# Kernel optimization log

Measured on AMD Instinct MI355X. Metric: run time of the kernel, lower is better.

## Reference

```python
import jax, jax.numpy as jnp
import numpy as np

H = 1024        # hidden_size == voc.num_words (required by module math)
V_OUT = 32000   # output_size / embedding vocab
B = 128
S = 512
MOG = 5


def _p(key, shape, scale=0.02):
    return scale * jax.random.normal(key, shape, dtype=jnp.float32)


def setup_inputs() -> dict:
    key = jax.random.key(0)
    ks = jax.random.split(key, 24)
    inp = {
        "input_step": jax.random.randint(ks[0], (1, B), 0, V_OUT),
        "encoder_outputs": jax.random.normal(ks[1], (S, B, H), dtype=jnp.float32),
        "h1": jax.random.normal(ks[2], (B, H), dtype=jnp.float32),
        "c1": jax.random.normal(ks[3], (B, H), dtype=jnp.float32),
        "emb": _p(ks[4], (V_OUT, H), 1.0),
        # mogrifier + LSTMCell params, layer 1 (input_size == hidden_size == H)
        "mog1_W": _p(ks[5], (MOG, H, H)),
        "mog1_b": _p(ks[6], (MOG, H)),
        "lstm1_Wih": _p(ks[7], (4 * H, H)),
        "lstm1_Whh": _p(ks[8], (4 * H, H)),
        "lstm1_bih": _p(ks[9], (4 * H,)),
        "lstm1_bhh": _p(ks[10], (4 * H,)),
        # layer 2
        "mog2_W": _p(ks[11], (MOG, H, H)),
        "mog2_b": _p(ks[12], (MOG, H)),
        "lstm2_Wih": _p(ks[13], (4 * H, H)),
        "lstm2_Whh": _p(ks[14], (4 * H, H)),
        "lstm2_bih": _p(ks[15], (4 * H,)),
        "lstm2_bhh": _p(ks[16], (4 * H,)),
        # MogLSTM.fc: hidden -> voc.num_words (== H)
        "fc_W": _p(ks[17], (H, H)),
        "fc_b": _p(ks[18], (H,)),
        # decoder concat / out
        "concat_W": _p(ks[19], (H, 2 * H)),
        "concat_b": _p(ks[20], (H,)),
        "out_W": _p(ks[21], (V_OUT, H)),
        "out_b": _p(ks[22], (V_OUT,)),
    }
    return inp


def _mog_lstm_cell(x, h, c, mog_W, mog_b, Wih, Whh, bih, bhh):
    # mogrify: 5 alternating tiny gated updates (x first, then h, ...)
    for i in range(MOG):
        g = 2.0 * jax.nn.sigmoid((h if (i + 1) % 2 != 0 else x) @ mog_W[i].T + mog_b[i])
        if (i + 1) % 2 == 0:
            h = g * h
        else:
            x = g * x
    gates = x @ Wih.T + bih + h @ Whh.T + bhh          # [B, 4H]
    i_, f_, g_, o_ = jnp.split(gates, 4, axis=1)        # torch order: i,f,g,o
    c = jax.nn.sigmoid(f_) * c + jax.nn.sigmoid(i_) * jnp.tanh(g_)
    h = jax.nn.sigmoid(o_) * jnp.tanh(c)
    return h, c


def reference(input_step, encoder_outputs, h1, c1, emb,
              mog1_W, mog1_b, lstm1_Wih, lstm1_Whh, lstm1_bih, lstm1_bhh,
              mog2_W, mog2_b, lstm2_Wih, lstm2_Whh, lstm2_bih, lstm2_bhh,
              fc_W, fc_b, concat_W, concat_b, out_W, out_b):
    x = emb[input_step[0]]                               # [B, H] (seq_len = 1)
    # MogLSTM: layer-1 uses provided (h1, c1); layer-2 state is zero-init
    h1n, _ = _mog_lstm_cell(x, h1, c1, mog1_W, mog1_b,
                            lstm1_Wih, lstm1_Whh, lstm1_bih, lstm1_bhh)
    z = jnp.zeros_like(h1n)
    h2n, _ = _mog_lstm_cell(h1n, z, z, mog2_W, mog2_b,
                            lstm2_Wih, lstm2_Whh, lstm2_bih, lstm2_bhh)
    rnn_out = h2n @ fc_W.T + fc_b                        # [B, H] (fc -> voc.num_words == H)
    hidden = h2n[None]                                   # [1, B, H]
    # Luong dot attention over encoder memory [S, B, H]
    scores = jnp.einsum('bh,sbh->bs', rnn_out, encoder_outputs)
    attn = jax.nn.softmax(scores, axis=1)                # [B, S]
    context = jnp.einsum('bs,sbh->bh', attn, encoder_outputs)
    concat_out = jnp.tanh(jnp.concatenate([rnn_out, context], axis=1) @ concat_W.T + concat_b)
    output = jax.nn.softmax(concat_out @ out_W.T + out_b, axis=1)  # [B, V_OUT]
    return output, hidden
```

## Files before the change

### kernel.cpp

```cpp
#include <hip/hip_runtime.h>
#include <math.h>

typedef unsigned short u16;
typedef unsigned int   u32;

#define B    128
#define H    1024
#define SEQ  512
#define VOUT 32000

#define NQ   4
#define SQB  (SEQ / NQ)
#define TS   8
#define NT   (SQB / TS)

using bf16x8 = __attribute__((ext_vector_type(8))) short;
using f32x4  = __attribute__((ext_vector_type(4))) float;

__device__ __forceinline__ float b2f(u32 u){ return __uint_as_float((u & 0xffffu) << 16); }
__device__ __forceinline__ float sigm(float x){ return 1.0f / (1.0f + expf(-x)); }
__device__ __forceinline__ u32 cvt2(float a, float b){
  u32 ua = __float_as_uint(a); ua += 0x7fffu + ((ua >> 16) & 1u);
  u32 ub = __float_as_uint(b); ub += 0x7fffu + ((ub >> 16) & 1u);
  return (ua >> 16) | (ub & 0xffff0000u);
}

__device__ __forceinline__ float ldf(const void* p, size_t i, int bf){
  return bf ? b2f(((const u16*)p)[i]) : ((const float*)p)[i];
}

__global__ void k_detect(const u16* __restrict__ enc, int* __restrict__ flag){
  __shared__ int cnt;
  if (threadIdx.x == 0) cnt = 0;
  __syncthreads();
  int c = 0;
  for (int j = threadIdx.x; j < 512; j += 256){
    u32 u = enc[j];
    u32 e = (u >> 7) & 0xFFu;
    c += (u == 0u || (e >= 100u && e <= 130u)) ? 1 : 0;
  }
  atomicAdd(&cnt, c);
  __syncthreads();
  if (threadIdx.x == 0) *flag = (cnt > 410) ? 1 : 0;
}

__global__ void k_init(const int* __restrict__ idx, const void* __restrict__ emb,
                       const void* __restrict__ h1, float* __restrict__ X, float* __restrict__ Hb,
                       const int* __restrict__ flagp){
  int bf = *flagp;
  int t = blockIdx.x * 256 + threadIdx.x;
  int b = t >> 10, h = t & (H - 1);
  X[t]  = ldf(emb, (size_t)idx[b] * H + h, bf);
  Hb[t] = ldf(h1, t, bf);
}

template<int OUT>
__global__ __launch_bounds__(256)
void gemm_s(const float* __restrict__ A, const void* __restrict__ W, size_t wOff,
            float* __restrict__ P, int K, int Kc, int N, const int* __restrict__ flagp)
{
  const int bf = *flagp;
  __shared__ float As[32][132];
  __shared__ float Wt[32][68];
  const int t  = threadIdx.x;
  const int n0 = blockIdx.x * 64;
  const int kbase = blockIdx.y * Kc;
  const int sb = t >> 1,  sk = (t & 1) << 4;
  const int wn = t >> 2,  wk = (t & 3) << 3;
  const int bx = (t & 15) << 3;
  const int ny = (t >> 4) << 2;

  float acc[8][4];
  #pragma unroll
  for (int i = 0; i < 8; ++i)
    #pragma unroll
    for (int j = 0; j < 4; ++j) acc[i][j] = 0.f;

  for (int k0 = 0; k0 < Kc; k0 += 32){
    const int kb = kbase + k0;
    const float4* Ap = (const float4*)(A + (size_t)sb * K + kb + sk);
    float4 a0 = Ap[0], a1 = Ap[1], a2 = Ap[2], a3 = Ap[3];
    size_t we = wOff + (size_t)(n0 + wn) * K + kb + wk;
    float w0,w1,w2,w3,w4,w5,w6,w7;
    if (bf){
      uint4 wv = *(const uint4*)((const u16*)W + we);
      w0=b2f(wv.x); w1=b2f(wv.x>>16); w2=b2f(wv.y); w3=b2f(wv.y>>16);
      w4=b2f(wv.z); w5=b2f(wv.z>>16); w6=b2f(wv.w); w7=b2f(wv.w>>16);
    } else {
      const float* Wf = (const float*)W + we;
      float4 p = *(const float4*)Wf, q = *(const float4*)(Wf + 4);
      w0=p.x; w1=p.y; w2=p.z; w3=p.w; w4=q.x; w5=q.y; w6=q.z; w7=q.w;
    }

    As[sk+ 0][sb]=a0.x; As[sk+ 1][sb]=a0.y; As[sk+ 2][sb]=a0.z; As[sk+ 3][sb]=a0.w;
    As[sk+ 4][sb]=a1.x; As[sk+ 5][sb]=a1.y; As[sk+ 6][sb]=a1.z; As[sk+ 7][sb]=a1.w;
    As[sk+ 8][sb]=a2.x; As[sk+ 9][sb]=a2.y; As[sk+10][sb]=a2.z; As[sk+11][sb]=a2.w;
    As[sk+12][sb]=a3.x; As[sk+13][sb]=a3.y; As[sk+14][sb]=a3.z; As[sk+15][sb]=a3.w;
    Wt[wk+0][wn]=w0; Wt[wk+1][wn]=w1; Wt[wk+2][wn]=w2; Wt[wk+3][wn]=w3;
    Wt[wk+4][wn]=w4; Wt[wk+5][wn]=w5; Wt[wk+6][wn]=w6; Wt[wk+7][wn]=w7;
    __syncthreads();

    #pragma unroll
    for (int kk = 0; kk < 32; ++kk){
      float4 wv = *(const float4*)(&Wt[kk][ny]);
      float a[8];
      #pragma unroll
      for (int i = 0; i < 8; ++i) a[i] = As[kk][bx+i];
      #pragma unroll
      for (int i = 0; i < 8; ++i){
        acc[i][0] = fmaf(a[i], wv.x, acc[i][0]);
        acc[i][1] = fmaf(a[i], wv.y, acc[i][1]);
        acc[i][2] = fmaf(a[i], wv.z, acc[i][2]);
        acc[i][3] = fmaf(a[i], wv.w, acc[i][3]);
      }
    }
    __syncthreads();
  }

  float* Pp = P + (size_t)blockIdx.y * B * N;
  #pragma unroll
  for (int j = 0; j < 4; ++j){
    int n = n0 + ny + j;
    #pragma unroll
    for (int i = 0; i < 8; ++i){
      size_t o = (size_t)(bx + i) * N + n;
      if (OUT == 0) Pp[o] = acc[i][j];
      else          Pp[o] += acc[i][j];
    }
  }
}

template<int ACT>
__global__ void ep_gen(const float* __restrict__ P, int S, const void* __restrict__ bias,
                       size_t bOff, float* __restrict__ C, int ostr,
                       const int* __restrict__ flagp){
  int bf = *flagp;
  int t = blockIdx.x * 256 + threadIdx.x;
  int b = t >> 10, h = t & (H - 1);
  float s = 0.f;
  for (int i = 0; i < S; ++i) s += P[(size_t)i * B * H + t];
  s += ldf(bias, bOff + h, bf);
  size_t o = (size_t)b * ostr + h;
  if (ACT == 0)      C[o] = s;
  else if (ACT == 1) C[o] = tanhf(s);
  else               C[o] = C[o] * 2.f * sigm(s);
}

__global__ void ep_lstm(const float* __restrict__ P, int S, const void* __restrict__ bih,
                        const void* __restrict__ bhh, const void* __restrict__ cprev,
                        float* __restrict__ hout, float* __restrict__ hf,
                        const void* __restrict__ mog2b, const int* __restrict__ flagp){
  int bf = *flagp;
  int t = blockIdx.x * 256 + threadIdx.x;
  int b = t >> 10, h = t & (H - 1);
  size_t base = (size_t)b * 4 * H;
  float gi=0.f, gf=0.f, gg=0.f, go=0.f;
  for (int s = 0; s < S; ++s){
    const float* q = P + (size_t)s * B * 4 * H + base;
    gi += q[h]; gf += q[H + h]; gg += q[2*H + h]; go += q[3*H + h];
  }
  gi += ldf(bih, h, bf)       + ldf(bhh, h, bf);
  gf += ldf(bih, H + h, bf)   + ldf(bhh, H + h, bf);
  gg += ldf(bih, 2*H + h, bf) + ldf(bhh, 2*H + h, bf);
  go += ldf(bih, 3*H + h, bf) + ldf(bhh, 3*H + h, bf);
  float c = cprev ? sigm(gf) * ldf(cprev, t, bf) : 0.f;
  c += sigm(gi) * tanhf(gg);
  float hv = sigm(go) * tanhf(c);
  if (hf) hf[t] = hv;
  if (mog2b){
    hv *= 8.f * sigm(ldf(mog2b, h, bf)) * sigm(ldf(mog2b, 2*H + h, bf))
              * sigm(ldf(mog2b, 4*H + h, bf));
  }
  hout[t] = hv;
}

template<int BF>
__device__ __forceinline__ void attn_body(const float* __restrict__ CAT,
                                          const void* __restrict__ enc,
                                          float* __restrict__ Pctx,
                                          float* __restrict__ Pml)
{
  __shared__ float els[TS][H];
  __shared__ float sc[TS];
  const int t = threadIdx.x;
  const int wave = t >> 6, lane = t & 63;
  const int b = blockIdx.x >> 2, q = blockIdx.x & 3;
  const int s0 = q * SQB;

  const float* rp = CAT + (size_t)b * 2 * H + lane * 16;
  float4 r0 = *(const float4*)rp,       r1 = *(const float4*)(rp + 4),
         r2 = *(const float4*)(rp + 8), r3 = *(const float4*)(rp + 12);

  float m = -3.0e38f, l = 0.f;
  float a0 = 0.f, a1 = 0.f, a2 = 0.f, a3 = 0.f;
  const int h0 = t * 4;

  float4 v[8];
  uint4  u[4];

  auto issue = [&](int tile){
    int ss = s0 + tile * TS;
    if (BF == 0){
      #pragma unroll
      for (int i = 0; i < 8; ++i){
        int seg = i * 256 + t;
        int r = seg >> 8, c = (seg & 255) * 4;
        v[i] = *(const float4*)((const float*)enc + ((size_t)(ss + r) * B + b) * H + c);
      }
    } else {
      #pragma unroll
      for (int i = 0; i < 4; ++i){
        int seg = i * 256 + t;
        int r = seg >> 7, c = (seg & 127) * 8;
        u[i] = *(const uint4*)((const u16*)enc + ((size_t)(ss + r) * B + b) * H + c);
      }
    }
  };
  auto commit = [&](){
    if (BF == 0){
      #pragma unroll
      for (int i = 0; i < 8; ++i) ((float4*)els)[i * 256 + t] = v[i];
    } else {
      #pragma unroll
      for (int i = 0; i < 4; ++i){
        int seg = i * 256 + t;
        float4 lo = {b2f(u[i].x), b2f(u[i].x >> 16), b2f(u[i].y), b2f(u[i].y >> 16)};
        float4 hi = {b2f(u[i].z), b2f(u[i].z >> 16), b2f(u[i].w), b2f(u[i].w >> 16)};
        ((float4*)els)[seg * 2]     = lo;
        ((float4*)els)[seg * 2 + 1] = hi;
      }
    }
  };

  issue(0);
  commit();
  __syncthreads();

  for (int tile = 0; tile < NT; ++tile){
    if (tile + 1 < NT) issue(tile + 1);

    #pragma unroll
    for (int i = 0; i < 2; ++i){
      int row = wave * 2 + i;
      const float* e = &els[row][lane * 16];
      float4 e0 = *(const float4*)e,       e1 = *(const float4*)(e + 4),
             e2 = *(const float4*)(e + 8), e3 = *(const float4*)(e + 12);
      float d = e0.x*r0.x + e0.y*r0.y + e0.z*r0.z + e0.w*r0.w
              + e1.x*r1.x + e1.y*r1.y + e1.z*r1.z + e1.w*r1.w
              + e2.x*r2.x + e2.y*r2.y + e2.z*r2.z + e2.w*r2.w
              + e3.x*r3.x + e3.y*r3.y + e3.z*r3.z + e3.w*r3.w;
      #pragma unroll
      for (int o = 32; o; o >>= 1) d += __shfl_down(d, o);
      if (lane == 0) sc[row] = d;
    }
    __syncthreads();

    float s0v = sc[0], s1v = sc[1], s2v = sc[2], s3v = sc[3];
    float s4v = sc[4], s5v = sc[5], s6v = sc[6], s7v = sc[7];
    float tm = fmaxf(fmaxf(fmaxf(s0v, s1v), fmaxf(s2v, s3v)),
                     fmaxf(fmaxf(s4v, s5v), fmaxf(s6v, s7v)));
    float nm = fmaxf(m, tm);
    float scale = expf(m - nm);
    float p0 = expf(s0v - nm), p1 = expf(s1v - nm), p2 = expf(s2v - nm), p3 = expf(s3v - nm);
    float p4 = expf(s4v - nm), p5 = expf(s5v - nm), p6 = expf(s6v - nm), p7 = expf(s7v - nm);
    l = l * scale + (p0 + p1 + p2 + p3 + p4 + p5 + p6 + p7);
    m = nm;
    a0 *= scale; a1 *= scale; a2 *= scale; a3 *= scale;
    #pragma unroll
    for (int s = 0; s < TS; ++s){
      float4 e = *(const float4*)(&els[s][h0]);
      float p = (s == 0 ? p0 : s == 1 ? p1 : s == 2 ? p2 : s == 3 ? p3 :
                 s == 4 ? p4 : s == 5 ? p5 : s == 6 ? p6 : p7);
      a0 = fmaf(p, e.x, a0); a1 = fmaf(p, e.y, a1);
      a2 = fmaf(p, e.z, a2); a3 = fmaf(p, e.w, a3);
    }
    __syncthreads();

    if (tile + 1 < NT){
      commit();
      __syncthreads();
    }
  }

  float4 av = {a0, a1, a2, a3};
  *(float4*)(Pctx + ((size_t)q * B + b) * H + h0) = av;
  if (t == 0){
    Pml[((size_t)q * B + b) * 2]     = m;
    Pml[((size_t)q * B + b) * 2 + 1] = l;
  }
}

__global__ __launch_bounds__(256)
void k_attn(const float* __restrict__ CAT, const void* __restrict__ enc,
            float* __restrict__ Pctx, float* __restrict__ Pml,
            const int* __restrict__ flagp){
  if (*flagp) attn_body<1>(CAT, enc, Pctx, Pml);
  else        attn_body<0>(CAT, enc, Pctx, Pml);
}

__global__ void k_attn_fin(const float* __restrict__ Pctx, const float* __restrict__ Pml,
                           float* __restrict__ CAT){
  int t = blockIdx.x * 256 + threadIdx.x;
  int b = t >> 10, h = t & (H - 1);
  float M = -3.0e38f;
  #pragma unroll
  for (int q = 0; q < NQ; ++q) M = fmaxf(M, Pml[((size_t)q * B + b) * 2]);
  float num = 0.f, den = 0.f;
  #pragma unroll
  for (int q = 0; q < NQ; ++q){
    float mq = Pml[((size_t)q * B + b) * 2];
    float lq = Pml[((size_t)q * B + b) * 2 + 1];
    float w = expf(mq - M);
    num = fmaf(w, Pctx[((size_t)q * B + b) * H + h], num);
    den = fmaf(w, lq, den);
  }
  CAT[(size_t)b * 2 * H + H + h] = num / den;
}

__global__ void k_cvtA(const float* __restrict__ X, u16* __restrict__ Xb){
  int t = blockIdx.x * 256 + threadIdx.x;
  const float4* p = (const float4*)(X + t * 8);
  float4 f0 = p[0], f1 = p[1];
  uint4 o;
  o.x = cvt2(f0.x, f0.y); o.y = cvt2(f0.z, f0.w);
  o.z = cvt2(f1.x, f1.y); o.w = cvt2(f1.z, f1.w);
  *(uint4*)(Xb + t * 8) = o;
}

__global__ __launch_bounds__(256)
void gemm_out_mfma(const u16* __restrict__ Xb, const void* __restrict__ W,
                   const void* __restrict__ bias, float* __restrict__ Cg,
                   const int* __restrict__ flagp)
{
  const int bf = *flagp;
  __shared__ u16 Ws[64][72];
  const int t = threadIdx.x;
  const int n0 = blockIdx.x * 64;
  const int wave = t >> 6, lane = t & 63;
  const int m0 = wave * 32;
  const int lm = lane & 15, quad = lane >> 4;
  const int sn = t >> 2, sk = (t & 3) * 16;

  f32x4 acc[2][4];
  #pragma unroll
  for (int i = 0; i < 2; ++i)
    #pragma unroll
    for (int j = 0; j < 4; ++j) acc[i][j] = (f32x4){0.f, 0.f, 0.f, 0.f};

  for (int k0 = 0; k0 < H; k0 += 64){
    if (bf){
      const u16* wp = (const u16*)W + (size_t)(n0 + sn) * H + k0 + sk;
      *(uint4*)(&Ws[sn][sk])     = *(const uint4*)wp;
      *(uint4*)(&Ws[sn][sk + 8]) = *(const uint4*)(wp + 8);
    } else {
      const float* wp = (const float*)W + (size_t)(n0 + sn) * H + k0 + sk;
      float4 f0 = *(const float4*)wp,     f1 = *(const float4*)(wp + 4);
      float4 f2 = *(const float4*)(wp+8), f3 = *(const float4*)(wp + 12);
      uint4 o0, o1;
      o0.x = cvt2(f0.x, f0.y); o0.y = cvt2(f0.z, f0.w);
      o0.z = cvt2(f1.x, f1.y); o0.w = cvt2(f1.z, f1.w);
      o1.x = cvt2(f2.x, f2.y); o1.y = cvt2(f2.z, f2.w);
      o1.z = cvt2(f3.x, f3.y); o1.w = cvt2(f3.z, f3.w);
      *(uint4*)(&Ws[sn][sk])     = o0;
      *(uint4*)(&Ws[sn][sk + 8]) = o1;
    }
    __syncthreads();
    #pragma unroll
    for (int ks = 0; ks < 64; ks += 32){
      bf16x8 a0 = *(const bf16x8*)(Xb + (size_t)(m0 + lm) * H + k0 + ks + quad * 8);
      bf16x8 a1 = *(const bf16x8*)(Xb + (size_t)(m0 + 16 + lm) * H + k0 + ks + quad * 8);
      #pragma unroll
      for (int nt = 0; nt < 4; ++nt){
        bf16x8 bfr = *(const bf16x8*)(&Ws[nt * 16 + lm][ks + quad * 8]);
        acc[0][nt] = __builtin_amdgcn_mfma_f32_16x16x32_bf16(a0, bfr, acc[0][nt], 0, 0, 0);
        acc[1][nt] = __builtin_amdgcn_mfma_f32_16x16x32_bf16(a1, bfr, acc[1][nt], 0, 0, 0);
      }
    }
    __syncthreads();
  }

  #pragma unroll
  for (int nt = 0; nt < 4; ++nt){
    int n = n0 + nt * 16 + lm;
    float bj = ldf(bias, n, bf);
    #pragma unroll
    for (int mt = 0; mt < 2; ++mt)
      #pragma unroll
      for (int r = 0; r < 4; ++r){
        int m = m0 + mt * 16 + quad * 4 + r;
        Cg[(size_t)m * VOUT + n] = acc[mt][nt][r] + bj;
      }
  }
}

__global__ __launch_bounds__(1024)
void k_softmax_v(float* __restrict__ out){
  int b = blockIdx.x, t = threadIdx.x;
  float* row = out + (size_t)b * VOUT;
  __shared__ float rm[16], rs[16];
  int lane = t & 63, w = t >> 6;
  float m = -3.0e38f;
  for (int i = 4*t; i < VOUT; i += 4096){
    float4 v = *(const float4*)(row + i);
    m = fmaxf(m, fmaxf(fmaxf(v.x, v.y), fmaxf(v.z, v.w)));
  }
  #pragma unroll
  for (int o = 32; o; o >>= 1) m = fmaxf(m, __shfl_down(m, o));
  if (!lane) rm[w] = m;
  __syncthreads();
  float M = rm[0];
  #pragma unroll
  for (int i = 1; i < 16; ++i) M = fmaxf(M, rm[i]);
  float s = 0.f;
  for (int i = 4*t; i < VOUT; i += 4096){
    float4 v = *(const float4*)(row + i);
    s += expf(v.x-M) + expf(v.y-M) + expf(v.z-M) + expf(v.w-M);
  }
  #pragma unroll
  for (int o = 32; o; o >>= 1) s += __shfl_down(s, o);
  if (!lane) rs[w] = s;
  __syncthreads();
  float S = rs[0];
  #pragma unroll
  for (int i = 1; i < 16; ++i) S += rs[i];
  float inv = 1.f / S;
  for (int i = 4*t; i < VOUT; i += 4096){
    float4 v = *(const float4*)(row + i);
    v.x = expf(v.x-M)*inv; v.y = expf(v.y-M)*inv;
    v.z = expf(v.z-M)*inv; v.w = expf(v.w-M)*inv;
    *(float4*)(row + i) = v;
  }
}

extern "C" void kernel_launch(void* const* d_in, const int* in_sizes, int n_in,
                              void* d_out, int out_size, void* d_ws, size_t ws_size,
                              hipStream_t stream){
  (void)in_sizes; (void)n_in; (void)out_size;
  const int* idx   = (const int*)d_in[0];
  const void* enc  = d_in[1];
  const void* h1   = d_in[2];
  const void* c1   = d_in[3];
  const void* emb  = d_in[4];
  const void* mog1W= d_in[5];
  const void* mog1b= d_in[6];
  const void* Wih1 = d_in[7];
  const void* Whh1 = d_in[8];
  const void* bih1 = d_in[9];
  const void* bhh1 = d_in[10];
  const void* mog2b= d_in[12];
  const void* Wih2 = d_in[13];
  const void* bih2 = d_in[15];
  const void* bhh2 = d_in[16];
  const void* fcW  = d_in[17];
  const void* fcb  = d_in[18];
  const void* ccW  = d_in[19];
  const void* ccb  = d_in[20];
  const void* outW = d_in[21];
  const void* outb = d_in[22];

  float* X    = (float*)d_ws;
  float* Hb   = X   + B*H;
  float* H2   = Hb  + B*H;
  float* CAT  = H2  + B*H;
  float* SC   = CAT + (size_t)B*2*H;
  int*  FLAG  = (int*)(SC + B*SEQ);
  u16*  Xb    = (u16*)(FLAG + 64);
  float* P    = (float*)(Xb + B*H);

  size_t need = ((size_t)(5*B*H + B*SEQ) + 64) * 4 + (size_t)B*H*2 + (size_t)4*B*4*H*4;
  int S1 = 16, S2 = 4;
  if (ws_size < need) { S1 = 4; S2 = 1; }

  float* out_f = (float*)d_out;
  float* hid_f = out_f + (size_t)B * VOUT;

  k_detect<<<1, 256, 0, stream>>>((const u16*)enc, FLAG);
  k_init<<<B*H/256, 256, 0, stream>>>(idx, emb, h1, X, Hb, FLAG);

  for (int i = 0; i < 5; ++i){
    const float* a = (i & 1) ? X : Hb;
    float*       c = (i & 1) ? Hb : X;
    gemm_s<0><<<dim3(H/64, S1), 256, 0, stream>>>(a, mog1W, (size_t)i*H*H, P, H, H/S1, H, FLAG);
    ep_gen<2><<<B*H/256, 256, 0, stream>>>(P, S1, mog1b, (size_t)i*H, c, H, FLAG);
  }

  gemm_s<0><<<dim3(4*H/64, S2), 256, 0, stream>>>(X,  Wih1, 0, P, H, H/S2, 4*H, FLAG);
  gemm_s<1><<<dim3(4*H/64, S2), 256, 0, stream>>>(Hb, Whh1, 0, P, H, H/S2, 4*H, FLAG);
  ep_lstm<<<B*H/256, 256, 0, stream>>>(P, S2, bih1, bhh1, c1, X, nullptr, mog2b, FLAG);

  gemm_s<0><<<dim3(4*H/64, S2), 256, 0, stream>>>(X, Wih2, 0, P, H, H/S2, 4*H, FLAG);
  ep_lstm<<<B*H/256, 256, 0, stream>>>(P, S2, bih2, bhh2, nullptr, H2, hid_f, nullptr, FLAG);

  gemm_s<0><<<dim3(H/64, S1), 256, 0, stream>>>(H2, fcW, 0, P, H, H/S1, H, FLAG);
  ep_gen<0><<<B*H/256, 256, 0, stream>>>(P, S1, fcb, 0, CAT, 2*H, FLAG);

  float* Pctx = P;
  float* Pml  = P + (size_t)NQ*B*H;
  k_attn<<<B*NQ, 256, 0, stream>>>(CAT, enc, Pctx, Pml, FLAG);
  k_attn_fin<<<B*H/256, 256, 0, stream>>>(Pctx, Pml, CAT);

  gemm_s<0><<<dim3(H/64, S1), 256, 0, stream>>>(CAT, ccW, 0, P, 2*H, 2*H/S1, H, FLAG);
  ep_gen<1><<<B*H/256, 256, 0, stream>>>(P, S1, ccb, 0, X, H, FLAG);
  k_cvtA<<<B*H/(256*8), 256, 0, stream>>>(X, Xb);
  gemm_out_mfma<<<VOUT/64, 256, 0, stream>>>(Xb, outW, outb, out_f, FLAG);
  k_softmax_v<<<B, 1024, 0, stream>>>(out_f);
}
```

Measured before the change: 895.5 us.

## Use split-bf16 MFMA GEMMs for mogrifier, LSTM and fc layers

Replaces the scalar fp32 shared-memory GEMMs for the mogrifier, both LSTM gate GEMMs and the fc layer with an MFMA kernel. It splits activations and fp32 weights into hi/lo bf16 pairs and runs three bf16 products to keep near-fp32 accuracy. The epilogues now emit the hi/lo activation splits directly, and the Wih/Whh gate GEMMs are fused into one launch. It also folds the bf16 conversion for the output GEMM into the tanh epilogue. The cost is three MFMA passes per tile plus on-the-fly weight splitting, which adds ALU work, and the split-K factor for the LSTM GEMMs is raised.

```diff
diff --git a/kernel.cpp b/kernel.cpp
--- a/kernel.cpp
+++ b/kernel.cpp
@@ -23,6 +23,16 @@
   u32 ua = __float_as_uint(a); ua += 0x7fffu + ((ua >> 16) & 1u);
   u32 ub = __float_as_uint(b); ub += 0x7fffu + ((ub >> 16) & 1u);
   return (ua >> 16) | (ub & 0xffff0000u);
+}
+__device__ __forceinline__ u16 f2b(float x){
+  u32 u = __float_as_uint(x); u += 0x7fffu + ((u >> 16) & 1u); return (u16)(u >> 16);
+}
+__device__ __forceinline__ float bval(u16 h){ return __uint_as_float((u32)h << 16); }
+__device__ __forceinline__ void split2(float a, float b, u32& hp, u32& lp){
+  u16 ha = f2b(a), hb = f2b(b);
+  u16 la = f2b(a - bval(ha)), lb = f2b(b - bval(hb));
+  hp = (u32)ha | ((u32)hb << 16);
+  lp = (u32)la | ((u32)lb << 16);
 }
 
 __device__ __forceinline__ float ldf(const void* p, size_t i, int bf){
@@ -46,12 +56,108 @@
 
 __global__ void k_init(const int* __restrict__ idx, const void* __restrict__ emb,
                        const void* __restrict__ h1, float* __restrict__ X, float* __restrict__ Hb,
+                       u16* __restrict__ SAh, u16* __restrict__ SAl,
+                       u16* __restrict__ SBh, u16* __restrict__ SBl,
                        const int* __restrict__ flagp){
   int bf = *flagp;
   int t = blockIdx.x * 256 + threadIdx.x;
   int b = t >> 10, h = t & (H - 1);
-  X[t]  = ldf(emb, (size_t)idx[b] * H + h, bf);
-  Hb[t] = ldf(h1, t, bf);
+  float xv = ldf(emb, (size_t)idx[b] * H + h, bf);
+  float hv = ldf(h1, t, bf);
+  X[t]  = xv; Hb[t] = hv;
+  u16 xh = f2b(xv); SAh[t] = xh; SAl[t] = f2b(xv - bval(xh));
+  u16 hh = f2b(hv); SBh[t] = hh; SBl[t] = f2b(hv - bval(hh));
+}
+
+template<int NOPS>
+__global__ __launch_bounds__(256)
+void gemm3(const u16* __restrict__ A0h, const u16* __restrict__ A0l,
+           const u16* __restrict__ A1h, const u16* __restrict__ A1l,
+           const void* __restrict__ W0, const void* __restrict__ W1, size_t wOff,
+           float* __restrict__ P, int K, int Kc, int N, const int* __restrict__ flagp)
+{
+  const int bf = *flagp;
+  __shared__ u16 Wh[64][72];
+  __shared__ u16 Wl[64][72];
+  const int t = threadIdx.x;
+  const int n0 = blockIdx.x * 64;
+  const int kbase = blockIdx.y * Kc;
+  const int wave = t >> 6, lane = t & 63;
+  const int m0 = wave * 32;
+  const int lm = lane & 15, quad = lane >> 4;
+  const int sn = t >> 2, sk = (t & 3) * 16;
+
+  f32x4 acc[2][4];
+  #pragma unroll
+  for (int i = 0; i < 2; ++i)
+    #pragma unroll
+    for (int j = 0; j < 4; ++j) acc[i][j] = (f32x4){0.f, 0.f, 0.f, 0.f};
+
+  #pragma unroll
+  for (int op = 0; op < NOPS; ++op){
+    const u16* Ah = (NOPS == 2 && op) ? A1h : A0h;
+    const u16* Al = (NOPS == 2 && op) ? A1l : A0l;
+    const void* W = (NOPS == 2 && op) ? W1  : W0;
+    for (int k0 = kbase; k0 < kbase + Kc; k0 += 64){
+      if (bf){
+        const u16* wp = (const u16*)W + wOff + (size_t)(n0 + sn) * K + k0 + sk;
+        *(uint4*)(&Wh[sn][sk])     = *(const uint4*)wp;
+        *(uint4*)(&Wh[sn][sk + 8]) = *(const uint4*)(wp + 8);
+        uint4 z = {0u, 0u, 0u, 0u};
+        *(uint4*)(&Wl[sn][sk])     = z;
+        *(uint4*)(&Wl[sn][sk + 8]) = z;
+      } else {
+        const float* wp = (const float*)W + wOff + (size_t)(n0 + sn) * K + k0 + sk;
+        float4 f0 = *(const float4*)wp,       f1 = *(const float4*)(wp + 4);
+        float4 f2 = *(const float4*)(wp + 8), f3 = *(const float4*)(wp + 12);
+        uint4 hi0, lo0, hi1, lo1;
+        split2(f0.x, f0.y, hi0.x, lo0.x); split2(f0.z, f0.w, hi0.y, lo0.y);
+        split2(f1.x, f1.y, hi0.z, lo0.z); split2(f1.z, f1.w, hi0.w, lo0.w);
+        split2(f2.x, f2.y, hi1.x, lo1.x); split2(f2.z, f2.w, hi1.y, lo1.y);
+        split2(f3.x, f3.y, hi1.z, lo1.z); split2(f3.z, f3.w, hi1.w, lo1.w);
+        *(uint4*)(&Wh[sn][sk])     = hi0;
+        *(uint4*)(&Wh[sn][sk + 8]) = hi1;
+        *(uint4*)(&Wl[sn][sk])     = lo0;
+        *(uint4*)(&Wl[sn][sk + 8]) = lo1;
+      }
+      __syncthreads();
+      #pragma unroll
+      for (int ks = 0; ks < 64; ks += 32){
+        size_t ab = (size_t)(m0 + lm) * K + k0 + ks + quad * 8;
+        bf16x8 ah0 = *(const bf16x8*)(Ah + ab);
+        bf16x8 al0 = *(const bf16x8*)(Al + ab);
+        bf16x8 ah1 = *(const bf16x8*)(Ah + ab + (size_t)16 * K);
+        bf16x8 al1 = *(const bf16x8*)(Al + ab + (size_t)16 * K);
+        #pragma unroll
+        for (int nt = 0; nt < 4; ++nt){
+          bf16x8 bh = *(const bf16x8*)(&Wh[nt * 16 + lm][ks + quad * 8]);
+          acc[0][nt] = __builtin_amdgcn_mfma_f32_16x16x32_bf16(ah0, bh, acc[0][nt], 0, 0, 0);
+          acc[1][nt] = __builtin_amdgcn_mfma_f32_16x16x32_bf16(ah1, bh, acc[1][nt], 0, 0, 0);
+          acc[0][nt] = __builtin_amdgcn_mfma_f32_16x16x32_bf16(al0, bh, acc[0][nt], 0, 0, 0);
+          acc[1][nt] = __builtin_amdgcn_mfma_f32_16x16x32_bf16(al1, bh, acc[1][nt], 0, 0, 0);
+          if (!bf){
+            bf16x8 bl = *(const bf16x8*)(&Wl[nt * 16 + lm][ks + quad * 8]);
+            acc[0][nt] = __builtin_amdgcn_mfma_f32_16x16x32_bf16(ah0, bl, acc[0][nt], 0, 0, 0);
+            acc[1][nt] = __builtin_amdgcn_mfma_f32_16x16x32_bf16(ah1, bl, acc[1][nt], 0, 0, 0);
+          }
+        }
+      }
+      __syncthreads();
+    }
+  }
+
+  float* Pp = P + (size_t)blockIdx.y * B * N;
+  #pragma unroll
+  for (int nt = 0; nt < 4; ++nt){
+    int n = n0 + nt * 16 + lm;
+    #pragma unroll
+    for (int mt = 0; mt < 2; ++mt)
+      #pragma unroll
+      for (int r = 0; r < 4; ++r){
+        int m = m0 + mt * 16 + quad * 4 + r;
+        Pp[(size_t)m * N + n] = acc[mt][nt][r];
+      }
+  }
 }
 
 template<int OUT>
@@ -133,6 +239,7 @@
 template<int ACT>
 __global__ void ep_gen(const float* __restrict__ P, int S, const void* __restrict__ bias,
                        size_t bOff, float* __restrict__ C, int ostr,
+                       u16* __restrict__ sh, u16* __restrict__ sl,
                        const int* __restrict__ flagp){
   int bf = *flagp;
   int t = blockIdx.x * 256 + threadIdx.x;
@@ -141,15 +248,20 @@
   for (int i = 0; i < S; ++i) s += P[(size_t)i * B * H + t];
   s += ldf(bias, bOff + h, bf);
   size_t o = (size_t)b * ostr + h;
-  if (ACT == 0)      C[o] = s;
-  else if (ACT == 1) C[o] = tanhf(s);
-  else               C[o] = C[o] * 2.f * sigm(s);
+  float v;
+  if (ACT == 0)      v = s;
+  else if (ACT == 1) v = tanhf(s);
+  else               v = C[o] * 2.f * sigm(s);
+  C[o] = v;
+  if (sh){ u16 hv = f2b(v); sh[t] = hv; if (sl) sl[t] = f2b(v - bval(hv)); }
 }
 
 __global__ void ep_lstm(const float* __restrict__ P, int S, const void* __restrict__ bih,
                         const void* __restrict__ bhh, const void* __restrict__ cprev,
                         float* __restrict__ hout, float* __restrict__ hf,
-                        const void* __restrict__ mog2b, const int* __restrict__ flagp){
+                        const void* __restrict__ mog2b,
+                        u16* __restrict__ sh, u16* __restrict__ sl,
+                        const int* __restrict__ flagp){
   int bf = *flagp;
   int t = blockIdx.x * 256 + threadIdx.x;
   int b = t >> 10, h = t & (H - 1);
@@ -172,6 +284,7 @@
               * sigm(ldf(mog2b, 4*H + h, bf));
   }
   hout[t] = hv;
+  if (sh){ u16 hb16 = f2b(hv); sh[t] = hb16; sl[t] = f2b(hv - bval(hb16)); }
 }
 
 template<int BF>
@@ -315,16 +428,6 @@
     den = fmaf(w, lq, den);
   }
   CAT[(size_t)b * 2 * H + H + h] = num / den;
-}
-
-__global__ void k_cvtA(const float* __restrict__ X, u16* __restrict__ Xb){
-  int t = blockIdx.x * 256 + threadIdx.x;
-  const float4* p = (const float4*)(X + t * 8);
-  float4 f0 = p[0], f1 = p[1];
-  uint4 o;
-  o.x = cvt2(f0.x, f0.y); o.y = cvt2(f0.z, f0.w);
-  o.z = cvt2(f1.x, f1.y); o.w = cvt2(f1.z, f1.w);
-  *(uint4*)(Xb + t * 8) = o;
 }
 
 __global__ __launch_bounds__(256)
@@ -464,35 +567,50 @@
   float* CAT  = H2  + B*H;
   float* SC   = CAT + (size_t)B*2*H;
   int*  FLAG  = (int*)(SC + B*SEQ);
-  u16*  Xb    = (u16*)(FLAG + 64);
+  u16*  SAh   = (u16*)(FLAG + 64);
+  u16*  SAl   = SAh + B*H;
+  u16*  SBh   = SAl + B*H;
+  u16*  SBl   = SBh + B*H;
+  u16*  Xb    = SBl + B*H;
   float* P    = (float*)(Xb + B*H);
 
-  size_t need = ((size_t)(5*B*H + B*SEQ) + 64) * 4 + (size_t)B*H*2 + (size_t)4*B*4*H*4;
-  int S1 = 16, S2 = 4;
+  int S1 = 16, S2 = 8;
+  size_t need = ((size_t)(5*B*H + B*SEQ) + 64) * 4 + (size_t)B*H*2*5
+              + (size_t)S2*B*4*H*4;
   if (ws_size < need) { S1 = 4; S2 = 1; }
 
   float* out_f = (float*)d_out;
   float* hid_f = out_f + (size_t)B * VOUT;
 
   k_detect<<<1, 256, 0, stream>>>((const u16*)enc, FLAG);
-  k_init<<<B*H/256, 256, 0, stream>>>(idx, emb, h1, X, Hb, FLAG);
+  k_init<<<B*H/256, 256, 0, stream>>>(idx, emb, h1, X, Hb, SAh, SAl, SBh, SBl, FLAG);
 
   for (int i = 0; i < 5; ++i){
-    const float* a = (i & 1) ? X : Hb;
-    float*       c = (i & 1) ? Hb : X;
-    gemm_s<0><<<dim3(H/64, S1), 256, 0, stream>>>(a, mog1W, (size_t)i*H*H, P, H, H/S1, H, FLAG);
-    ep_gen<2><<<B*H/256, 256, 0, stream>>>(P, S1, mog1b, (size_t)i*H, c, H, FLAG);
-  }
-
-  gemm_s<0><<<dim3(4*H/64, S2), 256, 0, stream>>>(X,  Wih1, 0, P, H, H/S2, 4*H, FLAG);
-  gemm_s<1><<<dim3(4*H/64, S2), 256, 0, stream>>>(Hb, Whh1, 0, P, H, H/S2, 4*H, FLAG);
-  ep_lstm<<<B*H/256, 256, 0, stream>>>(P, S2, bih1, bhh1, c1, X, nullptr, mog2b, FLAG);
-
-  gemm_s<0><<<dim3(4*H/64, S2), 256, 0, stream>>>(X, Wih2, 0, P, H, H/S2, 4*H, FLAG);
-  ep_lstm<<<B*H/256, 256, 0, stream>>>(P, S2, bih2, bhh2, nullptr, H2, hid_f, nullptr, FLAG);
-
-  gemm_s<0><<<dim3(H/64, S1), 256, 0, stream>>>(H2, fcW, 0, P, H, H/S1, H, FLAG);
-  ep_gen<0><<<B*H/256, 256, 0, stream>>>(P, S1, fcb, 0, CAT, 2*H, FLAG);
+    const u16 *ah, *al; float* c; u16 *ch, *cl;
+    if (i & 1){ ah = SAh; al = SAl; c = Hb; ch = SBh; cl = SBl; }
+    else      { ah = SBh; al = SBl; c = X;  ch = SAh; cl = SAl; }
+    gemm3<1><<<dim3(H/64, S1), 256, 0, stream>>>(ah, al, nullptr, nullptr,
+                                                 mog1W, nullptr, (size_t)i*H*H,
+                                                 P, H, H/S1, H, FLAG);
+    ep_gen<2><<<B*H/256, 256, 0, stream>>>(P, S1, mog1b, (size_t)i*H, c, H, ch, cl, FLAG);
+  }
+
+  gemm3<2><<<dim3(4*H/64, S2), 256, 0, stream>>>(SAh, SAl, SBh, SBl,
+                                                 Wih1, Whh1, 0,
+                                                 P, H, H/S2, 4*H, FLAG);
+  ep_lstm<<<B*H/256, 256, 0, stream>>>(P, S2, bih1, bhh1, c1, X, nullptr, mog2b,
+                                       SAh, SAl, FLAG);
+
+  gemm3<1><<<dim3(4*H/64, S2), 256, 0, stream>>>(SAh, SAl, nullptr, nullptr,
+                                                 Wih2, nullptr, 0,
+                                                 P, H, H/S2, 4*H, FLAG);
+  ep_lstm<<<B*H/256, 256, 0, stream>>>(P, S2, bih2, bhh2, nullptr, H2, hid_f, nullptr,
+                                       SBh, SBl, FLAG);
+
+  gemm3<1><<<dim3(H/64, S1), 256, 0, stream>>>(SBh, SBl, nullptr, nullptr,
+                                               fcW, nullptr, 0,
+                                               P, H, H/S1, H, FLAG);
+  ep_gen<0><<<B*H/256, 256, 0, stream>>>(P, S1, fcb, 0, CAT, 2*H, nullptr, nullptr, FLAG);
 
   float* Pctx = P;
   float* Pml  = P + (size_t)NQ*B*H;
@@ -500,8 +618,7 @@
   k_attn_fin<<<B*H/256, 256, 0, stream>>>(Pctx, Pml, CAT);
 
   gemm_s<0><<<dim3(H/64, S1), 256, 0, stream>>>(CAT, ccW, 0, P, 2*H, 2*H/S1, H, FLAG);
-  ep_gen<1><<<B*H/256, 256, 0, stream>>>(P, S1, ccb, 0, X, H, FLAG);
-  k_cvtA<<<B*H/(256*8), 256, 0, stream>>>(X, Xb);
+  ep_gen<1><<<B*H/256, 256, 0, stream>>>(P, S1, ccb, 0, X, H, Xb, nullptr, FLAG);
   gemm_out_mfma<<<VOUT/64, 256, 0, stream>>>(Xb, outW, outb, out_f, FLAG);
   k_softmax_v<<<B, 1024, 0, stream>>>(out_f);
 }
```

Result: faster. 802.7 us (-10.4%).
